# Kernel optimization log

Measured on AMD Instinct MI355X. Metric: run time of the kernel, lower is better.

The kernel has to match this reference:

```python
import jax, jax.numpy as jnp
import numpy as np

N = 50000
E = 1600000
DX = 128
DH = 128
DY = 64
NEG_SLOPE = 0.0  # in_neg_slope; LeakyReLU slope in GAT attention


def _init(key, shape, fan_in):
    return jax.random.normal(key, shape, dtype=jnp.float32) / np.sqrt(fan_in)


def setup_inputs() -> dict:
    key = jax.random.key(0)
    ks = jax.random.split(key, 12)
    node_x = jax.random.normal(ks[0], (N, DX), dtype=jnp.float32)
    edge_index = jax.random.randint(ks[1], (2, E), 0, N, dtype=jnp.int32)
    return {
        "node_x": node_x,
        "edge_index": edge_index,
        # GATConv layer 1 (DX -> DH, heads=1)
        "W1": _init(ks[2], (DX, DH), DX),
        "att_src1": _init(ks[3], (DH,), DH),
        "att_dst1": _init(ks[4], (DH,), DH),
        "b1": jnp.zeros((DH,), dtype=jnp.float32),
        # GATConv layer 2 (DH -> DH)
        "W2": _init(ks[5], (DH, DH), DH),
        "att_src2": _init(ks[6], (DH,), DH),
        "att_dst2": _init(ks[7], (DH,), DH),
        "b2": jnp.zeros((DH,), dtype=jnp.float32),
        # output Linear (DH -> DY)
        "W_out": _init(ks[8], (DH, DY), DH),
        "b_out": jnp.zeros((DY,), dtype=jnp.float32),
    }


def _gat_conv(x, src, dst, W, att_src, att_dst, bias, n):
    # h: [N, DH] transformed features
    h = x @ W
    # per-edge attention logits: a_src . h_j + a_dst . h_i
    e = (h @ att_src)[src] + (h @ att_dst)[dst]          # [E']
    e = jnp.where(e > 0, e, NEG_SLOPE * e)               # LeakyReLU
    # segment softmax over incoming edges of each destination node
    m = jax.lax.stop_gradient(jax.ops.segment_max(e, dst, num_segments=n))
    ex = jnp.exp(e - m[dst])
    denom = jax.ops.segment_sum(ex, dst, num_segments=n)
    alpha = ex / denom[dst]                              # [E']
    # scatter-add weighted source features to destinations
    out = jax.ops.segment_sum(h[src] * alpha[:, None], dst, num_segments=n)
    return out + bias


def reference(node_x, edge_index, W1, att_src1, att_dst1, b1,
              W2, att_src2, att_dst2, b2, W_out, b_out):
    n = node_x.shape[0]
    src, dst = edge_index[0], edge_index[1]
    # PyG GATConv default add_self_loops=True
    loop = jnp.arange(n, dtype=src.dtype)
    src = jnp.concatenate([src, loop])
    dst = jnp.concatenate([dst, loop])
    x1 = jax.nn.relu(_gat_conv(node_x, src, dst, W1, att_src1, att_dst1, b1, n))
    x2 = _gat_conv(x1, src, dst, W2, att_src2, att_dst2, b2, n)
    return x2 @ W_out + b_out
```

## Files before the change

kernel.cpp:

```cpp
#include <hip/hip_runtime.h>
#include <hip/hip_fp16.h>

typedef unsigned short u16;
typedef unsigned int   u32;
typedef _Float16 f16;
typedef __attribute__((ext_vector_type(8))) f16 f16x8;
typedef __attribute__((ext_vector_type(2))) f16 h2;
typedef __attribute__((ext_vector_type(4))) float f32x4;

#define NN 50000
#define EE 1600000
#define DD 128
#define DYY 64
#define NB 196
#define EPB 8192
#define GB 196
#define MAXD 160
#define NTILE 3125
#define GMM 782
#define XST 144

__device__ __forceinline__ u16 f2h(float f){
  union { f16 h; u16 u; } x; x.h = (f16)f; return x.u;
}
__device__ __forceinline__ float wave_sum(float v){
  #pragma unroll
  for (int s = 32; s; s >>= 1) v += __shfl_xor(v, s, 64);
  return v;
}

__device__ __forceinline__ void wfrag_one(const float* __restrict__ W, u16* __restrict__ Wf,
                                          int nct, int s){
  int lane = s & 63;
  int t  = (s >> 6) % nct;
  int ks = (s >> 6) / nct;
  int q = lane >> 4, n = lane & 15;
  int N = nct * 16;
  u16 tmp[8];
  #pragma unroll
  for (int j = 0; j < 8; ++j)
    tmp[j] = f2h(W[(ks * 32 + q * 8 + j) * N + t * 16 + n]);
  *(uint4*)(Wf + (size_t)s * 8) = *(const uint4*)tmp;
}

__global__ __launch_bounds__(256) void kA_prep(const int* __restrict__ dst, int* __restrict__ hist2d,
                                               const float* __restrict__ W1, const float* __restrict__ W2,
                                               const float* __restrict__ Wo,
                                               const float* __restrict__ b2, const float* __restrict__ bo,
                                               u16* __restrict__ Wf1, u16* __restrict__ Wf2,
                                               u16* __restrict__ Wfo, float* __restrict__ c64){
  int b = blockIdx.x, tid = threadIdx.x;
  if (b < GB){
    __shared__ int hist[256];
    hist[tid] = 0;
    __syncthreads();
    int e0 = b * EPB, e1 = min(e0 + EPB, EE);
    for (int e = e0 + tid; e < e1; e += 256) atomicAdd(&hist[dst[e] >> 8], 1);
    __syncthreads();
    hist2d[b * 256 + tid] = hist[tid];
  } else if (b < 204) wfrag_one(W1, Wf1, 8, (b - 196) * 256 + tid);
  else if (b < 212)   wfrag_one(W2, Wf2, 8, (b - 204) * 256 + tid);
  else if (b < 216)   wfrag_one(Wo, Wfo, 4, (b - 212) * 256 + tid);
  else if (tid < DYY){
    float s = bo[tid];
    for (int k = 0; k < DD; ++k) s += b2[k] * Wo[k * DYY + tid];
    c64[tid] = s;
  }
}

__device__ __forceinline__ void gemm_tile(const float* __restrict__ X,
                                          const u16* __restrict__ Wf, u16* __restrict__ Hout,
                                          const float* __restrict__ as, const float* __restrict__ ad,
                                          float* __restrict__ Sv, float* __restrict__ Dv,
                                          int blk, int tid, uint4* Wl){
  const uint4* Wg = (const uint4*)Wf;
  #pragma unroll
  for (int i = 0; i < 8; ++i) Wl[tid + 256 * i] = Wg[tid + 256 * i];
  __syncthreads();
  int wv = tid >> 6, lane = tid & 63;
  int rtile = blk * 4 + wv;
  if (rtile >= NTILE) return;
  int q = lane >> 4, n = lane & 15;
  int arow = rtile * 16 + n;
  f32x4 acc[8];
  #pragma unroll
  for (int t = 0; t < 8; ++t) acc[t] = (f32x4){0.f, 0.f, 0.f, 0.f};
  union F8 { uint4 u; f16x8 v; f16 h[8]; };
  #pragma unroll
  for (int ks = 0; ks < 4; ++ks){
    int kb = ks * 32 + q * 8;
    const float* xp = X + (size_t)arow * DD + kb;
    float4 f0 = *(const float4*)xp;
    float4 f1 = *(const float4*)(xp + 4);
    F8 a;
    a.h[0] = (f16)f0.x; a.h[1] = (f16)f0.y; a.h[2] = (f16)f0.z; a.h[3] = (f16)f0.w;
    a.h[4] = (f16)f1.x; a.h[5] = (f16)f1.y; a.h[6] = (f16)f1.z; a.h[7] = (f16)f1.w;
    #pragma unroll
    for (int t = 0; t < 8; ++t){
      F8 b; b.u = Wl[(ks * 8 + t) * 64 + lane];
      acc[t] = __builtin_amdgcn_mfma_f32_16x16x32_f16(a.v, b.v, acc[t], 0, 0, 0);
    }
  }
  float ps[4] = {0, 0, 0, 0}, pd[4] = {0, 0, 0, 0};
  #pragma unroll
  for (int t = 0; t < 8; ++t){
    float a_s = as[t * 16 + n];
    float a_d = ad[t * 16 + n];
    #pragma unroll
    for (int rg = 0; rg < 4; ++rg){
      ps[rg] += acc[t][rg] * a_s;
      pd[rg] += acc[t][rg] * a_d;
    }
  }
  #pragma unroll
  for (int rg = 0; rg < 4; ++rg){
    #pragma unroll
    for (int s = 1; s < 16; s <<= 1){
      ps[rg] += __shfl_xor(ps[rg], s, 64);
      pd[rg] += __shfl_xor(pd[rg], s, 64);
    }
  }
  #pragma unroll
  for (int rg = 0; rg < 4; ++rg){
    int grow = rtile * 16 + q * 4 + rg;
    if (n == 0){ Sv[grow] = ps[rg]; Dv[grow] = pd[rg]; }
    #pragma unroll
    for (int t = 0; t < 8; ++t)
      Hout[(size_t)grow * DD + t * 16 + n] = f2h(acc[t][rg]);
  }
}

__global__ __launch_bounds__(256) void kBC(const int* __restrict__ src, const int* __restrict__ dst,
                                           const int* __restrict__ hist2d,
                                           int* __restrict__ btot, int* __restrict__ bbase,
                                           u32* __restrict__ buf,
                                           const float* __restrict__ X0, const u16* __restrict__ Wf1,
                                           u16* __restrict__ Hbf1,
                                           const float* __restrict__ as1, const float* __restrict__ ad1,
                                           float* __restrict__ Sv1, float* __restrict__ Dv1){
  __shared__ __align__(16) uint4 Wl[2048];
  int b = blockIdx.x, tid = threadIdx.x;
  if (b < GB){
    int* lcur = (int*)Wl;
    int* sd   = ((int*)Wl) + 256;
    int c = b;
    int pre = 0, tot = 0;
    for (int cc = 0; cc < GB; ++cc){
      int v = hist2d[cc * 256 + tid];
      if (cc < c) pre += v;
      tot += v;
    }
    sd[tid] = tot;
    __syncthreads();
    for (int o = 1; o < 256; o <<= 1){
      int t = (tid >= o) ? sd[tid - o] : 0;
      __syncthreads();
      sd[tid] += t;
      __syncthreads();
    }
    int bb = sd[tid] - tot;
    if (c == 0){ btot[tid] = tot; bbase[tid] = bb; }
    lcur[tid] = bb + pre;
    __syncthreads();
    int e0 = c * EPB, e1 = min(e0 + EPB, EE);
    for (int e = e0 + tid; e < e1; e += 256){
      int d = dst[e];
      int pos = atomicAdd(&lcur[d >> 8], 1);
      buf[pos] = (u32)src[e] | ((u32)(d & 255) << 16);
    }
  } else {
    gemm_tile(X0, Wf1, Hbf1, as1, ad1, Sv1, Dv1, b - GB, tid, Wl);
  }
}

__global__ __launch_bounds__(256) void kD_finalize(const u32* __restrict__ buf,
                                                   const int* __restrict__ btot, const int* __restrict__ bbase,
                                                   int* __restrict__ offs, int* __restrict__ cnt,
                                                   u16* __restrict__ srcs){
  __shared__ int dh[256];
  __shared__ int sd[256];
  __shared__ int dcur[256];
  int tid = threadIdx.x, b = blockIdx.x;
  int n = btot[b], base = bbase[b];
  dh[tid] = 0;
  __syncthreads();
  for (int i = tid; i < n; i += 256) atomicAdd(&dh[(buf[base + i] >> 16) & 255], 1);
  __syncthreads();
  int v = dh[tid];
  sd[tid] = v;
  __syncthreads();
  for (int o = 1; o < 256; o <<= 1){
    int t = (tid >= o) ? sd[tid - o] : 0;
    __syncthreads();
    sd[tid] += t;
    __syncthreads();
  }
  int excl = sd[tid] - v;
  dcur[tid] = base + excl;
  int d = (b << 8) + tid;
  if (d < NN){ offs[d] = base + excl; cnt[d] = v; }
  __syncthreads();
  for (int i = tid; i < n; i += 256){
    u32 u = buf[base + i];
    int pos = atomicAdd(&dcur[(u >> 16) & 255], 1);
    srcs[pos] = (u16)(u & 0xffffu);
  }
}

__device__ void agg_node_lds(const u16* __restrict__ H, const float* __restrict__ Sv,
                             const float* __restrict__ Dv, const int* __restrict__ offs,
                             const int* __restrict__ cnt, const u16* __restrict__ srcs,
                             const float* __restrict__ bias, u16* __restrict__ xrow,
                             int do_relu, int wid, int lane, int* si, float* sw){
  int off = offs[wid], c = cnt[wid];
  float dvw = Dv[wid];
  float wself = __expf(fmaxf(Sv[wid] + dvw, 0.f));
  int cf = min(c, MAXD);
  int grp = lane >> 4, cg_ = lane & 15;
  const u32* H32 = (const u32*)H;
  union F8 { uint4 u; h2 p[4]; };
  F8 rself; rself.u = (uint4){0, 0, 0, 0};
  if (grp == 0) rself.u = *(const uint4*)(H32 + (size_t)wid * 64 + cg_ * 4);
  float dl = 0.f;
  for (int j = lane; j < c; j += 64){
    int sidx = (int)srcs[off + j];
    float wgt = __expf(fmaxf(Sv[sidx] + dvw, 0.f));
    if (j < MAXD){ si[j] = sidx; sw[j] = wgt; }
    dl += wgt;
  }
  float inv = 1.f / (wave_sum(dl) + wself);
  h2 accA[4] = {(h2){0,0},(h2){0,0},(h2){0,0},(h2){0,0}};
  h2 accB[4] = {(h2){0,0},(h2){0,0},(h2){0,0},(h2){0,0}};
  if (grp == 0){
    f16 wh = (f16)(wself * inv); h2 w2 = {wh, wh};
    #pragma unroll
    for (int i = 0; i < 4; ++i) accA[i] = rself.p[i] * w2;
  }
  int base = 0;
  int nfull = cf & ~7;
  for (; base < nfull; base += 8){
    int j0 = base + grp, j1 = j0 + 4;
    int s0 = si[j0], s1 = si[j1];
    float w0 = sw[j0] * inv, w1 = sw[j1] * inv;
    F8 r0; r0.u = *(const uint4*)(H32 + (size_t)s0 * 64 + cg_ * 4);
    F8 r1; r1.u = *(const uint4*)(H32 + (size_t)s1 * 64 + cg_ * 4);
    f16 wh0 = (f16)w0; h2 w20 = {wh0, wh0};
    f16 wh1 = (f16)w1; h2 w21 = {wh1, wh1};
    #pragma unroll
    for (int i = 0; i < 4; ++i){
      accA[i] += r0.p[i] * w20;
      accB[i] += r1.p[i] * w21;
    }
  }
  for (; base < cf; base += 4){
    int j = base + grp;
    float wgt = 0.f; int sidx = 0;
    if (j < cf){ wgt = sw[j] * inv; sidx = si[j]; }
    f16 wh = (f16)wgt; h2 w2 = {wh, wh};
    F8 r; r.u = *(const uint4*)(H32 + (size_t)sidx * 64 + cg_ * 4);
    #pragma unroll
    for (int i = 0; i < 4; ++i) accA[i] += r.p[i] * w2;
  }
  for (int base2 = MAXD; base2 < c; base2 += 4){
    int j = base2 + grp;
    bool valid = j < c;
    int sidx = valid ? (int)srcs[off + j] : 0;
    float wgt = valid ? __expf(fmaxf(Sv[sidx] + dvw, 0.f)) * inv : 0.f;
    f16 wh = (f16)wgt; h2 w2 = {wh, wh};
    F8 r; r.u = *(const uint4*)(H32 + (size_t)sidx * 64 + cg_ * 4);
    #pragma unroll
    for (int i = 0; i < 4; ++i) accA[i] += r.p[i] * w2;
  }
  #pragma unroll
  for (int i = 0; i < 4; ++i) accA[i] += accB[i];
  union FU { h2 v; float f; };
  #pragma unroll
  for (int i = 0; i < 4; ++i){
    FU a; a.v = accA[i];
    FU o1; o1.f = __shfl_xor(a.f, 16, 64); a.v = a.v + o1.v;
    FU o2; o2.f = __shfl_xor(a.f, 32, 64); a.v = a.v + o2.v;
    accA[i] = a.v;
  }
  if (grp == 0){
    uint4 pk;
    u32* pkp = (u32*)&pk;
    #pragma unroll
    for (int qq = 0; qq < 4; ++qq){
      float o0 = (float)accA[qq].x + bias[cg_ * 8 + 2 * qq];
      float o1 = (float)accA[qq].y + bias[cg_ * 8 + 2 * qq + 1];
      if (do_relu){ o0 = fmaxf(o0, 0.f); o1 = fmaxf(o1, 0.f); }
      pkp[qq] = ((u32)f2h(o1) << 16) | (u32)f2h(o0);
    }
    *(uint4*)(xrow + cg_ * 8) = pk;
  }
}

__global__ __launch_bounds__(256, 8) void kE(const u16* __restrict__ Hbf1,
                                          const float* __restrict__ Sv1, const float* __restrict__ Dv1,
                                          const int* __restrict__ offs, const int* __restrict__ cnt,
                                          const u16* __restrict__ srcs, const float* __restrict__ b1,
                                          const u16* __restrict__ Wf2, const u16* __restrict__ Wfo,
                                          const float* __restrict__ as2, const float* __restrict__ ad2,
                                          u16* __restrict__ G2,
                                          float* __restrict__ Sv2, float* __restrict__ Dv2){
  __shared__ __align__(16) u16 Xs[16 * XST];
  __shared__ int   s_i[4][MAXD];
  __shared__ float s_w[4][MAXD];
  __shared__ float svp[16], dvp[16];
  int tid = threadIdx.x, wv = tid >> 6, lane = tid & 63;
  int rtile = blockIdx.x;
  if (tid < 16){ svp[tid] = 0.f; dvp[tid] = 0.f; }
  #pragma unroll
  for (int k = 0; k < 4; ++k){
    int r = wv * 4 + k;
    agg_node_lds(Hbf1, Sv1, Dv1, offs, cnt, srcs, b1, Xs + r * XST, 1,
                 rtile * 16 + r, lane, s_i[wv], s_w[wv]);
  }
  __syncthreads();
  const uint4* Wg = (const uint4*)Wf2;
  int q = lane >> 4, n = lane & 15;
  f32x4 acc[2] = {(f32x4){0.f,0.f,0.f,0.f}, (f32x4){0.f,0.f,0.f,0.f}};
  union F8 { uint4 u; f16x8 v; };
  #pragma unroll
  for (int ks = 0; ks < 4; ++ks){
    F8 a; a.u = *(const uint4*)((const char*)Xs + n * (XST * 2) + ks * 64 + q * 16);
    #pragma unroll
    for (int tt = 0; tt < 2; ++tt){
      F8 b; b.u = Wg[(ks * 8 + wv * 2 + tt) * 64 + lane];
      acc[tt] = __builtin_amdgcn_mfma_f32_16x16x32_f16(a.v, b.v, acc[tt], 0, 0, 0);
    }
  }
  float ps[4] = {0, 0, 0, 0}, pd[4] = {0, 0, 0, 0};
  #pragma unroll
  for (int tt = 0; tt < 2; ++tt){
    int t = wv * 2 + tt;
    float a_s = as2[t * 16 + n];
    float a_d = ad2[t * 16 + n];
    #pragma unroll
    for (int rg = 0; rg < 4; ++rg){
      ps[rg] += acc[tt][rg] * a_s;
      pd[rg] += acc[tt][rg] * a_d;
    }
  }
  #pragma unroll
  for (int rg = 0; rg < 4; ++rg){
    #pragma unroll
    for (int s = 1; s < 16; s <<= 1){
      ps[rg] += __shfl_xor(ps[rg], s, 64);
      pd[rg] += __shfl_xor(pd[rg], s, 64);
    }
  }
  if (n == 0){
    #pragma unroll
    for (int rg = 0; rg < 4; ++rg){
      atomicAdd(&svp[q * 4 + rg], ps[rg]);
      atomicAdd(&dvp[q * 4 + rg], pd[rg]);
    }
  }
  __syncthreads();
  if (tid < 16){ Sv2[rtile * 16 + tid] = svp[tid]; Dv2[rtile * 16 + tid] = dvp[tid]; }
  #pragma unroll
  for (int tt = 0; tt < 2; ++tt)
    #pragma unroll
    for (int rg = 0; rg < 4; ++rg)
      Xs[(q * 4 + rg) * XST + (wv * 2 + tt) * 16 + n] = f2h(acc[tt][rg]);
  __syncthreads();
  const uint4* Wo4 = (const uint4*)Wfo;
  f32x4 g = (f32x4){0.f, 0.f, 0.f, 0.f};
  #pragma unroll
  for (int ks = 0; ks < 4; ++ks){
    F8 a; a.u = *(const uint4*)((const char*)Xs + n * (XST * 2) + ks * 64 + q * 16);
    F8 b; b.u = Wo4[(ks * 4 + wv) * 64 + lane];
    g = __builtin_amdgcn_mfma_f32_16x16x32_f16(a.v, b.v, g, 0, 0, 0);
  }
  #pragma unroll
  for (int rg = 0; rg < 4; ++rg){
    int grow = rtile * 16 + q * 4 + rg;
    G2[(size_t)grow * DYY + wv * 16 + n] = f2h(g[rg]);
  }
}

__device__ void agg_node_out(const u16* __restrict__ G2v, const float* __restrict__ Sv,
                             const float* __restrict__ Dv, const int* __restrict__ offs,
                             const int* __restrict__ cnt, const u16* __restrict__ srcs,
                             const float* __restrict__ c64, float* __restrict__ out,
                             int wid, int lane, int* si, float* sw){
  int off = offs[wid], c = cnt[wid];
  float dvw = Dv[wid];
  float wself = __expf(fmaxf(Sv[wid] + dvw, 0.f));
  int cf = min(c, MAXD);
  int grp = lane >> 3, cg_ = lane & 7;
  const u32* G = (const u32*)G2v;
  union F8 { uint4 u; h2 p[4]; };
  F8 rself; rself.u = (uint4){0, 0, 0, 0};
  if (grp == 0) rself.u = *(const uint4*)(G + (size_t)wid * 32 + cg_ * 4);
  float dl = 0.f;
  for (int j = lane; j < c; j += 64){
    int sidx = (int)srcs[off + j];
    float wgt = __expf(fmaxf(Sv[sidx] + dvw, 0.f));
    if (j < MAXD){ si[j] = sidx; sw[j] = wgt; }
    dl += wgt;
  }
  float inv = 1.f / (wave_sum(dl) + wself);
  h2 accA[4] = {(h2){0,0},(h2){0,0},(h2){0,0},(h2){0,0}};
  h2 accB[4] = {(h2){0,0},(h2){0,0},(h2){0,0},(h2){0,0}};
  if (grp == 0){
    f16 wh = (f16)(wself * inv); h2 w2 = {wh, wh};
    #pragma unroll
    for (int i = 0; i < 4; ++i) accA[i] = rself.p[i] * w2;
  }
  int base = 0;
  int nfull = cf & ~15;
  for (; base < nfull; base += 16){
    int j0 = base + grp, j1 = j0 + 8;
    int s0 = si[j0], s1 = si[j1];
    float w0 = sw[j0] * inv, w1 = sw[j1] * inv;
    F8 r0; r0.u = *(const uint4*)(G + (size_t)s0 * 32 + cg_ * 4);
    F8 r1; r1.u = *(const uint4*)(G + (size_t)s1 * 32 + cg_ * 4);
    f16 wh0 = (f16)w0; h2 x0 = {wh0, wh0};
    f16 wh1 = (f16)w1; h2 x1 = {wh1, wh1};
    #pragma unroll
    for (int i = 0; i < 4; ++i){
      accA[i] += r0.p[i] * x0;
      accB[i] += r1.p[i] * x1;
    }
  }
  for (; base < cf; base += 8){
    int j = base + grp;
    float wgt = 0.f; int sidx = 0;
    if (j < cf){ wgt = sw[j] * inv; sidx = si[j]; }
    f16 wh = (f16)wgt; h2 w2 = {wh, wh};
    F8 r; r.u = *(const uint4*)(G + (size_t)sidx * 32 + cg_ * 4);
    #pragma unroll
    for (int i = 0; i < 4; ++i) accA[i] += r.p[i] * w2;
  }
  for (int b2i = MAXD; b2i < c; b2i += 8){
    int j = b2i + grp;
    bool valid = j < c;
    int sidx = valid ? (int)srcs[off + j] : 0;
    float wgt = valid ? __expf(fmaxf(Sv[sidx] + dvw, 0.f)) * inv : 0.f;
    F8 r; r.u = *(const uint4*)(G + (size_t)sidx * 32 + cg_ * 4);
    f16 wh = (f16)wgt; h2 w2 = {wh, wh};
    #pragma unroll
    for (int i = 0; i < 4; ++i) accA[i] += r.p[i] * w2;
  }
  #pragma unroll
  for (int i = 0; i < 4; ++i) accA[i] += accB[i];
  union FU { h2 v; float f; };
  #pragma unroll
  for (int i = 0; i < 4; ++i){
    FU a; a.v = accA[i];
    FU o1; o1.f = __shfl_xor(a.f,  8, 64); a.v = a.v + o1.v;
    FU o2; o2.f = __shfl_xor(a.f, 16, 64); a.v = a.v + o2.v;
    FU o3; o3.f = __shfl_xor(a.f, 32, 64); a.v = a.v + o3.v;
    accA[i] = a.v;
  }
  if (grp == 0){
    float4 o0, o1v;
    const float4* cv = (const float4*)(c64 + cg_ * 8);
    o0.x = (float)accA[0].x + cv[0].x;
    o0.y = (float)accA[0].y + cv[0].y;
    o0.z = (float)accA[1].x + cv[0].z;
    o0.w = (float)accA[1].y + cv[0].w;
    o1v.x = (float)accA[2].x + cv[1].x;
    o1v.y = (float)accA[2].y + cv[1].y;
    o1v.z = (float)accA[3].x + cv[1].z;
    o1v.w = (float)accA[3].y + cv[1].w;
    float4* op = (float4*)(out + (size_t)wid * DYY + cg_ * 8);
    op[0] = o0; op[1] = o1v;
  }
}

__global__ __launch_bounds__(256, 8) void kF(const u16* __restrict__ G2,
                                          const float* __restrict__ Sv2, const float* __restrict__ Dv2,
                                          const int* __restrict__ offs, const int* __restrict__ cnt,
                                          const u16* __restrict__ srcs,
                                          const float* __restrict__ c64,
                                          float* __restrict__ out){
  __shared__ int   s_i[4][MAXD];
  __shared__ float s_w[4][MAXD];
  int tid = threadIdx.x, wv = tid >> 6, lane = tid & 63;
  int rtile = blockIdx.x;
  #pragma unroll
  for (int k = 0; k < 4; ++k)
    agg_node_out(G2, Sv2, Dv2, offs, cnt, srcs, c64, out,
                 rtile * 16 + wv * 4 + k, lane, s_i[wv], s_w[wv]);
}

extern "C" void kernel_launch(void* const* d_in, const int* in_sizes, int n_in,
                              void* d_out, int out_size, void* d_ws, size_t ws_size,
                              hipStream_t stream) {
  const float* node_x = (const float*)d_in[0];
  const int* ei   = (const int*)d_in[1];
  const int* srcp = ei;
  const int* dstp = ei + EE;
  const float* W1  = (const float*)d_in[2];
  const float* as1 = (const float*)d_in[3];
  const float* ad1 = (const float*)d_in[4];
  const float* b1  = (const float*)d_in[5];
  const float* W2  = (const float*)d_in[6];
  const float* as2 = (const float*)d_in[7];
  const float* ad2 = (const float*)d_in[8];
  const float* b2  = (const float*)d_in[9];
  const float* Wo  = (const float*)d_in[10];
  const float* bo  = (const float*)d_in[11];

  char* w = (char*)d_ws;
  u16*   Hbf1  = (u16*)w;  w += (size_t)NN * DD * 2;
  u32*   buf   = (u32*)w;
  u16*   G2    = (u16*)w;  w += (size_t)EE * 4;
  float* Sv1   = (float*)w; w += (size_t)NN * 4;
  float* Dv1   = (float*)w; w += (size_t)NN * 4;
  float* Sv2   = (float*)w; w += (size_t)NN * 4;
  float* Dv2   = (float*)w; w += (size_t)NN * 4;
  int*   cnt   = (int*)w;   w += (size_t)NN * 4;
  int*   offs  = (int*)w;   w += (size_t)NN * 4;
  int*   btot  = (int*)w;   w += 1024;
  int*   bbase = (int*)w;   w += 1024;
  int*   hist2d = (int*)w;  w += GB * 256 * 4;
  u16*   srcs  = (u16*)w;   w += (size_t)EE * 2;
  u16*   Wf1   = (u16*)w;   w += 32768;
  u16*   Wf2   = (u16*)w;   w += 32768;
  u16*   Wfo   = (u16*)w;   w += 16384;
  float* c64   = (float*)w; w += 256;

  const int TB = 256;

  kA_prep    <<<217,      TB, 0, stream>>>(dstp, hist2d, W1, W2, Wo, b2, bo,
                                           Wf1, Wf2, Wfo, c64);
  kBC        <<<GB + GMM, TB, 0, stream>>>(srcp, dstp, hist2d, btot, bbase, buf,
                                           node_x, Wf1, Hbf1, as1, ad1, Sv1, Dv1);
  kD_finalize<<<NB,       TB, 0, stream>>>(buf, btot, bbase, offs, cnt, srcs);
  kE         <<<NTILE,    TB, 0, stream>>>(Hbf1, Sv1, Dv1, offs, cnt, srcs, b1,
                                           Wf2, Wfo, as2, ad2, G2, Sv2, Dv2);
  kF         <<<NTILE,    TB, 0, stream>>>(G2, Sv2, Dv2, offs, cnt, srcs, c64,
                                           (float*)d_out);
}
```

Baseline: 240.6 us.

## Widen kE to 8 waves per tile and give kF one node per wave

kE now runs 512 threads per 16-row tile. Each wave aggregates 2 nodes instead of 4 and computes one 16-column MFMA tile of the layer-2 transform, and only the first 4 waves do the output projection. kF launches 12500 blocks with one destination node per wave instead of looping over 4 nodes per wave. Both changes aim to expose more parallelism and cut the serial per-wave latency of the gather loops. The cost is more LDS per kE block, idle waves during the output GEMM, and more block-launch overhead in kF.

```diff
diff --git a/kernel.cpp b/kernel.cpp
--- a/kernel.cpp
+++ b/kernel.cpp
@@ -17,6 +17,7 @@
 #define GB 196
 #define MAXD 160
 #define NTILE 3125
+#define NFB 12500
 #define GMM 782
 #define XST 144
 
@@ -295,7 +296,7 @@
   }
 }
 
-__global__ __launch_bounds__(256, 8) void kE(const u16* __restrict__ Hbf1,
+__global__ __launch_bounds__(512, 8) void kE(const u16* __restrict__ Hbf1,
                                           const float* __restrict__ Sv1, const float* __restrict__ Dv1,
                                           const int* __restrict__ offs, const int* __restrict__ cnt,
                                           const u16* __restrict__ srcs, const float* __restrict__ b1,
@@ -304,42 +305,37 @@
                                           u16* __restrict__ G2,
                                           float* __restrict__ Sv2, float* __restrict__ Dv2){
   __shared__ __align__(16) u16 Xs[16 * XST];
-  __shared__ int   s_i[4][MAXD];
-  __shared__ float s_w[4][MAXD];
+  __shared__ int   s_i[8][MAXD];
+  __shared__ float s_w[8][MAXD];
   __shared__ float svp[16], dvp[16];
   int tid = threadIdx.x, wv = tid >> 6, lane = tid & 63;
   int rtile = blockIdx.x;
   if (tid < 16){ svp[tid] = 0.f; dvp[tid] = 0.f; }
   #pragma unroll
-  for (int k = 0; k < 4; ++k){
-    int r = wv * 4 + k;
+  for (int k = 0; k < 2; ++k){
+    int r = wv * 2 + k;
     agg_node_lds(Hbf1, Sv1, Dv1, offs, cnt, srcs, b1, Xs + r * XST, 1,
                  rtile * 16 + r, lane, s_i[wv], s_w[wv]);
   }
   __syncthreads();
   const uint4* Wg = (const uint4*)Wf2;
   int q = lane >> 4, n = lane & 15;
-  f32x4 acc[2] = {(f32x4){0.f,0.f,0.f,0.f}, (f32x4){0.f,0.f,0.f,0.f}};
+  f32x4 acc = (f32x4){0.f, 0.f, 0.f, 0.f};
   union F8 { uint4 u; f16x8 v; };
   #pragma unroll
   for (int ks = 0; ks < 4; ++ks){
     F8 a; a.u = *(const uint4*)((const char*)Xs + n * (XST * 2) + ks * 64 + q * 16);
-    #pragma unroll
-    for (int tt = 0; tt < 2; ++tt){
-      F8 b; b.u = Wg[(ks * 8 + wv * 2 + tt) * 64 + lane];
-      acc[tt] = __builtin_amdgcn_mfma_f32_16x16x32_f16(a.v, b.v, acc[tt], 0, 0, 0);
-    }
-  }
-  float ps[4] = {0, 0, 0, 0}, pd[4] = {0, 0, 0, 0};
-  #pragma unroll
-  for (int tt = 0; tt < 2; ++tt){
-    int t = wv * 2 + tt;
-    float a_s = as2[t * 16 + n];
-    float a_d = ad2[t * 16 + n];
+    F8 b; b.u = Wg[(ks * 8 + wv) * 64 + lane];
+    acc = __builtin_amdgcn_mfma_f32_16x16x32_f16(a.v, b.v, acc, 0, 0, 0);
+  }
+  float ps[4], pd[4];
+  {
+    float a_s = as2[wv * 16 + n];
+    float a_d = ad2[wv * 16 + n];
     #pragma unroll
     for (int rg = 0; rg < 4; ++rg){
-      ps[rg] += acc[tt][rg] * a_s;
-      pd[rg] += acc[tt][rg] * a_d;
+      ps[rg] = acc[rg] * a_s;
+      pd[rg] = acc[rg] * a_d;
     }
   }
   #pragma unroll
@@ -360,23 +356,23 @@
   __syncthreads();
   if (tid < 16){ Sv2[rtile * 16 + tid] = svp[tid]; Dv2[rtile * 16 + tid] = dvp[tid]; }
   #pragma unroll
-  for (int tt = 0; tt < 2; ++tt)
-    #pragma unroll
-    for (int rg = 0; rg < 4; ++rg)
-      Xs[(q * 4 + rg) * XST + (wv * 2 + tt) * 16 + n] = f2h(acc[tt][rg]);
-  __syncthreads();
-  const uint4* Wo4 = (const uint4*)Wfo;
-  f32x4 g = (f32x4){0.f, 0.f, 0.f, 0.f};
-  #pragma unroll
-  for (int ks = 0; ks < 4; ++ks){
-    F8 a; a.u = *(const uint4*)((const char*)Xs + n * (XST * 2) + ks * 64 + q * 16);
-    F8 b; b.u = Wo4[(ks * 4 + wv) * 64 + lane];
-    g = __builtin_amdgcn_mfma_f32_16x16x32_f16(a.v, b.v, g, 0, 0, 0);
-  }
-  #pragma unroll
-  for (int rg = 0; rg < 4; ++rg){
-    int grow = rtile * 16 + q * 4 + rg;
-    G2[(size_t)grow * DYY + wv * 16 + n] = f2h(g[rg]);
+  for (int rg = 0; rg < 4; ++rg)
+    Xs[(q * 4 + rg) * XST + wv * 16 + n] = f2h(acc[rg]);
+  __syncthreads();
+  if (wv < 4){
+    const uint4* Wo4 = (const uint4*)Wfo;
+    f32x4 g = (f32x4){0.f, 0.f, 0.f, 0.f};
+    #pragma unroll
+    for (int ks = 0; ks < 4; ++ks){
+      F8 a; a.u = *(const uint4*)((const char*)Xs + n * (XST * 2) + ks * 64 + q * 16);
+      F8 b; b.u = Wo4[(ks * 4 + wv) * 64 + lane];
+      g = __builtin_amdgcn_mfma_f32_16x16x32_f16(a.v, b.v, g, 0, 0, 0);
+    }
+    #pragma unroll
+    for (int rg = 0; rg < 4; ++rg){
+      int grow = rtile * 16 + q * 4 + rg;
+      G2[(size_t)grow * DYY + wv * 16 + n] = f2h(g[rg]);
+    }
   }
 }
 
@@ -480,11 +476,8 @@
   __shared__ int   s_i[4][MAXD];
   __shared__ float s_w[4][MAXD];
   int tid = threadIdx.x, wv = tid >> 6, lane = tid & 63;
-  int rtile = blockIdx.x;
-  #pragma unroll
-  for (int k = 0; k < 4; ++k)
-    agg_node_out(G2, Sv2, Dv2, offs, cnt, srcs, c64, out,
-                 rtile * 16 + wv * 4 + k, lane, s_i[wv], s_w[wv]);
+  agg_node_out(G2, Sv2, Dv2, offs, cnt, srcs, c64, out,
+               blockIdx.x * 4 + wv, lane, s_i[wv], s_w[wv]);
 }
 
 extern "C" void kernel_launch(void* const* d_in, const int* in_sizes, int n_in,
@@ -531,8 +524,8 @@
   kBC        <<<GB + GMM, TB, 0, stream>>>(srcp, dstp, hist2d, btot, bbase, buf,
                                            node_x, Wf1, Hbf1, as1, ad1, Sv1, Dv1);
   kD_finalize<<<NB,       TB, 0, stream>>>(buf, btot, bbase, offs, cnt, srcs);
-  kE         <<<NTILE,    TB, 0, stream>>>(Hbf1, Sv1, Dv1, offs, cnt, srcs, b1,
+  kE         <<<NTILE,   512, 0, stream>>>(Hbf1, Sv1, Dv1, offs, cnt, srcs, b1,
                                            Wf2, Wfo, as2, ad2, G2, Sv2, Dv2);
-  kF         <<<NTILE,    TB, 0, stream>>>(G2, Sv2, Dv2, offs, cnt, srcs, c64,
+  kF         <<<NFB,      TB, 0, stream>>>(G2, Sv2, Dv2, offs, cnt, srcs, c64,
                                            (float*)d_out);
 }
```

Measured after the change: 243.2 us. Within noise of the previous version (+1.1%).
